# Optimization experiments

Measured on AMD Instinct MI355X. Metric: run time of the kernel, lower is better.

The kernel has to match this reference:

```python
import jax, jax.numpy as jnp
import numpy as np

NUM_CAPS = 8
NITER = 3
TAU = 1.0
N_NODES = 50000
N_EDGES = 800000
D_FEAT = 128


def _l2norm(v):
    # matches torch fn.normalize(dim=-1, eps=1e-12): v / max(||v||, eps)
    n = jnp.linalg.norm(v, axis=-1, keepdims=True)
    return v / jnp.maximum(n, 1e-12)


def setup_inputs() -> dict:
    key = jax.random.key(0)
    k1, k2, k3 = jax.random.split(key, 3)
    x = jax.random.normal(k1, (N_NODES, D_FEAT), dtype=jnp.float32)
    src = jax.random.randint(k2, (N_EDGES,), 0, N_NODES)
    trg = jax.random.randint(k3, (N_EDGES,), 0, N_NODES)
    edge_index = jnp.stack([src, trg], axis=0).astype(jnp.int64)
    return {"x": x, "edge_index": edge_index}


def reference(x, edge_index):
    num_node, num_dim = x.shape
    dpc = num_dim // NUM_CAPS  # dim per capsule
    src, trg = edge_index[0], edge_index[1]

    xc = _l2norm(x.reshape(num_node, NUM_CAPS, dpc))  # [N, C, d]
    z = xc[src]                                        # [E, C, d] gathered source caps
    u = xc
    for _ in range(NITER):
        # per-edge, per-capsule agreement score
        p = jnp.einsum('ecd,ecd->ec', z, u[trg])       # [E, C]
        p = jax.nn.softmax(p / TAU, axis=1)
        msg = z * p[:, :, None]                        # [E, C, d]
        u = jax.ops.segment_sum(msg, trg, num_segments=num_node)  # [N, C, d]
        u = _l2norm(u + xc)
    return u.reshape(num_node, num_dim)
```

## Files before the change

kernel.cpp:

```cpp
#include <hip/hip_runtime.h>
#include <hip/hip_bf16.h>

#define DF   128
#define DPC  16
#define KCAP 64

#define NB_XC    2048
#define NB_BKT   2048
#define NB_ROUTE 1536
#define NB_ZERO  64

__device__ __forceinline__ float cap_sum(float v) {
    v += __shfl_xor(v, 1);
    v += __shfl_xor(v, 2);
    v += __shfl_xor(v, 4);
    return v;
}
__device__ __forceinline__ float bits_lo(unsigned int w) {
    union { unsigned int u; float f; } c; c.u = w << 16; return c.f;
}
__device__ __forceinline__ float bits_hi(unsigned int w) {
    union { unsigned int u; float f; } c; c.u = w & 0xFFFF0000u; return c.f;
}
__device__ __forceinline__ unsigned int f2b_pack(float lo, float hi) {
    __hip_bfloat16 a = __float2bfloat16(lo), b = __float2bfloat16(hi);
    unsigned short ua = *reinterpret_cast<unsigned short*>(&a);
    unsigned short ub = *reinterpret_cast<unsigned short*>(&b);
    return ((unsigned int)ub << 16) | ua;
}
__device__ __forceinline__ float2 load_x2(const void* __restrict__ xraw, int fp32,
                                          int node, int lane) {
    size_t off = (size_t)node * DF + (size_t)lane * 2;
    if (fp32) {
        return *reinterpret_cast<const float2*>((const float*)xraw + off);
    } else {
        unsigned int w = ((const unsigned int*)xraw)[(size_t)node * 64 + lane];
        return make_float2(bits_lo(w), bits_hi(w));
    }
}
__device__ __forceinline__ void proc_pk(const uint4& w0, const uint4& w1,
                                        bool valid, const float* u, float* acc) {
    unsigned ww[8] = {w0.x, w0.y, w0.z, w0.w, w1.x, w1.y, w1.z, w1.w};
    float p = 0.0f;
    #pragma unroll
    for (int q = 0; q < 8; ++q) {
        p = fmaf(bits_lo(ww[q]), u[2*q],   p);
        p = fmaf(bits_hi(ww[q]), u[2*q+1], p);
    }
    float ex = __expf(p);
    float sd = ex;
    sd += __shfl_xor(sd, 1);
    sd += __shfl_xor(sd, 2);
    sd += __shfl_xor(sd, 4);
    float w = valid ? ex * __builtin_amdgcn_rcpf(sd) : 0.0f;
    #pragma unroll
    for (int q = 0; q < 8; ++q) {
        acc[2*q]   = fmaf(w, bits_lo(ww[q]), acc[2*q]);
        acc[2*q+1] = fmaf(w, bits_hi(ww[q]), acc[2*q+1]);
    }
}

__global__ void k_detect_zero(const unsigned int* __restrict__ xw,
                              const unsigned int* __restrict__ ew,
                              int* __restrict__ flags, int* __restrict__ cnt,
                              int zwords) {
    if (blockIdx.x == 0) {
        __shared__ int s_nan, s_zero;
        int tid = threadIdx.x;
        if (tid == 0) { s_nan = 0; s_zero = 0; }
        __syncthreads();
        int cnt_nan = 0;
        for (int i = tid; i < 4096; i += 256) {
            unsigned int lo = xw[i] & 0xFFFFu;
            if ((lo & 0x7F80u) == 0x7F80u) cnt_nan++;
        }
        int cnt_zero = 0;
        for (int i = tid; i < 1024; i += 256) {
            if (ew[2 * i + 1] == 0u) cnt_zero++;
        }
        atomicAdd(&s_nan, cnt_nan);
        atomicAdd(&s_zero, cnt_zero);
        __syncthreads();
        if (tid == 0) {
            flags[0] = (s_nan > 0) ? 1 : 0;
            flags[1] = (s_zero > 512) ? 1 : 0;
        }
    } else {
        int stride = (NB_ZERO - 1) * 256;
        for (int i = (blockIdx.x - 1) * 256 + threadIdx.x; i < zwords; i += stride)
            cnt[i] = 0;
    }
}

__global__ void k_xc(const void* __restrict__ xraw,
                     unsigned int* __restrict__ xcb,
                     const int* __restrict__ flags, int n_nodes) {
    const int fp32 = flags[0];
    const int lane = threadIdx.x & 63;
    const int gw   = (blockIdx.x * blockDim.x + threadIdx.x) >> 6;
    const int nw   = (gridDim.x * blockDim.x) >> 6;
    for (int wid = gw; wid < n_nodes; wid += nw) {
        float2 v = load_x2(xraw, fp32, wid, lane);
        float ss = cap_sum(v.x * v.x + v.y * v.y);
        float scale = 1.0f / fmaxf(sqrtf(ss), 1e-12f);
        int cc = lane >> 3, jp = lane & 7;
        int w = (jp < 4) ? (cc * 4 + jp) : (32 + cc * 4 + (jp - 4));
        xcb[(size_t)wid * 64 + w] = f2b_pack(v.x * scale, v.y * scale);
    }
}

__global__ void k_bucket(const int* __restrict__ ei,
                         int* __restrict__ cnt, int cstr,
                         unsigned short* __restrict__ rows,
                         const int* __restrict__ flags,
                         int n_nodes, int n_edges) {
    const int i64 = flags[1];
    const int gtid = blockIdx.x * blockDim.x + threadIdx.x;
    const int gth  = gridDim.x * blockDim.x;
    for (int e = gtid; e < n_edges; e += gth) {
        int s, t;
        if (i64) {
            long sv = ((const long*)ei)[e];
            long tv = ((const long*)ei)[(size_t)n_edges + e];
            s = (int)sv; t = (int)tv;
        } else {
            s = ei[e]; t = ei[(size_t)n_edges + e];
        }
        if ((unsigned)s < (unsigned)n_nodes && (unsigned)t < (unsigned)n_nodes) {
            int slot = atomicAdd(cnt + (size_t)t * cstr, 1);
            if (slot < KCAP)
                rows[(size_t)t * KCAP + slot] = (unsigned short)s;
        }
    }
}

__global__ void __launch_bounds__(256)
__attribute__((amdgpu_waves_per_eu(8)))
k_route(const unsigned short* __restrict__ rows,
        const unsigned int* __restrict__ xcb,
        const int* __restrict__ cnt, int cstr,
        float* __restrict__ u_out, int n_nodes) {
    __shared__ char smem[4 * 6144];
    const int lane = threadIdx.x & 63;
    char* wbase = smem + (threadIdx.x >> 6) * 6144;
    const int gw = (blockIdx.x * blockDim.x + threadIdx.x) >> 6;
    const int nw = (gridDim.x * blockDim.x) >> 6;
    const int e8 = lane >> 3;
    const int c  = lane & 7;
    const int coff = c * 16;
    const char* __restrict__ xb = (const char*)xcb;

    for (int t = gw; t < n_nodes; t += nw) {
        const unsigned* wrow = (const unsigned*)(rows + (size_t)t * KCAP);
        unsigned rw = wrow[lane & 31];
        int deg = cnt[(size_t)t * cstr];
        deg = __builtin_amdgcn_readfirstlane(deg);
        deg = min(deg, KCAP);

        size_t trow = (size_t)t << 8;
        uint4 t0 = *reinterpret_cast<const uint4*>(xb + trow + coff);
        uint4 t1 = *reinterpret_cast<const uint4*>(xb + trow + 128 + coff);

        auto nid = [&](int s) -> int {
            unsigned wv = __shfl(rw, (lane & 32) | (s >> 1));
            return (int)((s & 1) ? (wv >> 16) : (wv & 0xFFFFu));
        };

        if (deg > 0) {
            int kmax = (min(deg, 24) + 7) >> 3;
            for (int k = 0; k < kmax; ++k) {
                int s  = e8 + 8 * k;
                int sl = (s < deg) ? s : 0;
                int off = nid(sl) << 8;
                const char* ga = xb + off + coff;
                const char* gb = ga + 128;
                __builtin_amdgcn_global_load_lds(
                    (const __attribute__((address_space(1))) unsigned int*)ga,
                    (__attribute__((address_space(3))) unsigned int*)
                        (wbase + k * 2048 + (lane << 4)), 16, 0, 0);
                __builtin_amdgcn_global_load_lds(
                    (const __attribute__((address_space(1))) unsigned int*)gb,
                    (__attribute__((address_space(3))) unsigned int*)
                        (wbase + k * 2048 + 1024 + (lane << 4)), 16, 0, 0);
            }
        }

        unsigned tw[8] = {t0.x, t0.y, t0.z, t0.w, t1.x, t1.y, t1.z, t1.w};
        float ss = 0.0f;
        #pragma unroll
        for (int q = 0; q < 8; ++q) {
            float xl = bits_lo(tw[q]), xh = bits_hi(tw[q]);
            ss = fmaf(xl, xl, ss);
            ss = fmaf(xh, xh, ss);
        }
        float sc = __builtin_amdgcn_rsqf(fmaxf(ss, 1e-24f));
        float u[DPC];
        #pragma unroll
        for (int q = 0; q < 8; ++q) {
            u[2*q]   = bits_lo(tw[q]) * sc;
            u[2*q+1] = bits_hi(tw[q]) * sc;
        }

        asm volatile("s_waitcnt vmcnt(0)" ::: "memory");

        for (int it = 0; it < 3; ++it) {
            asm volatile("" ::: "memory");

            float acc[DPC];
            #pragma unroll
            for (int j = 0; j < DPC; ++j) acc[j] = 0.0f;

            #pragma unroll
            for (int k = 0; k < 3; ++k) {
                if (deg > 8 * k) {
                    uint4 a = *reinterpret_cast<const uint4*>(
                        wbase + k * 2048 + (lane << 4));
                    uint4 b = *reinterpret_cast<const uint4*>(
                        wbase + k * 2048 + 1024 + (lane << 4));
                    proc_pk(a, b, 8 * k + e8 < deg, u, acc);
                }
            }
            if (deg > 24) {
                for (int base = 24; base < deg; base += 8) {
                    int s  = base + e8;
                    int sl = (s < deg) ? s : 0;
                    int off = nid(sl) << 8;
                    uint4 a = *reinterpret_cast<const uint4*>(xb + off + coff);
                    uint4 b = *reinterpret_cast<const uint4*>(xb + off + 128 + coff);
                    proc_pk(a, b, s < deg, u, acc);
                }
            }

            #pragma unroll
            for (int j = 0; j < DPC; ++j) {
                acc[j] += __shfl_xor(acc[j], 8);
                acc[j] += __shfl_xor(acc[j], 16);
                acc[j] += __shfl_xor(acc[j], 32);
            }
            float s2 = 0.0f;
            #pragma unroll
            for (int q = 0; q < 8; ++q) {
                float xl = bits_lo(tw[q]) * sc;
                float xh = bits_hi(tw[q]) * sc;
                u[2*q]   = acc[2*q]   + xl;
                u[2*q+1] = acc[2*q+1] + xh;
                s2 = fmaf(u[2*q],   u[2*q],   s2);
                s2 = fmaf(u[2*q+1], u[2*q+1], s2);
            }
            float sc2 = __builtin_amdgcn_rsqf(fmaxf(s2, 1e-24f));
            #pragma unroll
            for (int j = 0; j < DPC; ++j) u[j] *= sc2;
        }

        if (e8 == 0) {
            float* dst = u_out + (size_t)t * DF + c * DPC;
            #pragma unroll
            for (int j = 0; j < DPC; j += 4)
                *reinterpret_cast<float4*>(dst + j) =
                    make_float4(u[j], u[j+1], u[j+2], u[j+3]);
        }
    }
}

extern "C" void kernel_launch(void* const* d_in, const int* in_sizes, int n_in,
                              void* d_out, int out_size, void* d_ws, size_t ws_size,
                              hipStream_t stream) {
    const void* x  = d_in[0];
    const int*  ei = (const int*)d_in[1];
    const int n_nodes = in_sizes[0] / DF;
    const int n_edges = in_sizes[1] / 2;
    const size_t NC = (size_t)n_nodes * DF;

    unsigned char* p = (unsigned char*)d_ws;
    unsigned int*   xcb  = (unsigned int*)p;   p += NC * 2;
    unsigned short* rows = (unsigned short*)p; p += (size_t)n_nodes * KCAP * 2;
    int*            flags = (int*)p;           p += 128;
    int*            cnt  = (int*)p;
    size_t used  = (size_t)(p - (unsigned char*)d_ws);
    size_t avail = (ws_size > used) ? (ws_size - used) : 0;
    int cstr = 32;
    while (cstr > 1 && (size_t)n_nodes * cstr * sizeof(int) > avail) cstr >>= 1;
    int zwords = n_nodes * cstr;

    float* u_out = (float*)d_out;

    k_detect_zero<<<NB_ZERO, 256, 0, stream>>>(
        (const unsigned int*)x, (const unsigned int*)ei, flags, cnt, zwords);
    k_bucket<<<NB_BKT, 256, 0, stream>>>(ei, cnt, cstr, rows, flags,
                                         n_nodes, n_edges);
    k_xc<<<NB_XC, 256, 0, stream>>>(x, xcb, flags, n_nodes);
    k_route<<<NB_ROUTE, 256, 0, stream>>>(rows, xcb, cnt, cstr, u_out, n_nodes);
}
```

Before: 262.7 us.

## Process two nodes per wave in routing, drop LDS staging, fuse prep kernels

The routing kernel now gives each half-wave its own target node, with 4 edges per pass instead of 8, so low-degree nodes waste fewer lanes. The global-to-LDS staging is replaced by direct global loads of the first 16 neighbours, software-pipelined two at a time and re-read each iteration. The xc normalization and edge bucketing kernels are merged into one launch, and the route grid and waves-per-EU hint are retuned. The cost is re-fetching neighbour rows from cache on every iteration, plus per-half-wave degree divergence, since each wave loops to the larger of its two degrees.

```diff
diff --git a/kernel.cpp b/kernel.cpp
--- a/kernel.cpp
+++ b/kernel.cpp
@@ -4,10 +4,10 @@
 #define DF   128
 #define DPC  16
 #define KCAP 64
-
-#define NB_XC    2048
-#define NB_BKT   2048
-#define NB_ROUTE 1536
+#define RWU  64
+
+#define NB_PREP  2048
+#define NB_ROUTE 1792
 #define NB_ZERO  64
 
 __device__ __forceinline__ float cap_sum(float v) {
@@ -92,9 +92,12 @@
     }
 }
 
-__global__ void k_xc(const void* __restrict__ xraw,
-                     unsigned int* __restrict__ xcb,
-                     const int* __restrict__ flags, int n_nodes) {
+__global__ void k_prep(const void* __restrict__ xraw, unsigned int* __restrict__ xcb,
+                       const int* __restrict__ ei,
+                       int* __restrict__ cnt, int cstr,
+                       unsigned short* __restrict__ rows,
+                       const int* __restrict__ flags,
+                       int n_nodes, int n_edges) {
     const int fp32 = flags[0];
     const int lane = threadIdx.x & 63;
     const int gw   = (blockIdx.x * blockDim.x + threadIdx.x) >> 6;
@@ -107,22 +110,15 @@
         int w = (jp < 4) ? (cc * 4 + jp) : (32 + cc * 4 + (jp - 4));
         xcb[(size_t)wid * 64 + w] = f2b_pack(v.x * scale, v.y * scale);
     }
-}
-
-__global__ void k_bucket(const int* __restrict__ ei,
-                         int* __restrict__ cnt, int cstr,
-                         unsigned short* __restrict__ rows,
-                         const int* __restrict__ flags,
-                         int n_nodes, int n_edges) {
+
     const int i64 = flags[1];
     const int gtid = blockIdx.x * blockDim.x + threadIdx.x;
     const int gth  = gridDim.x * blockDim.x;
     for (int e = gtid; e < n_edges; e += gth) {
         int s, t;
         if (i64) {
-            long sv = ((const long*)ei)[e];
-            long tv = ((const long*)ei)[(size_t)n_edges + e];
-            s = (int)sv; t = (int)tv;
+            s = (int)((const long long*)ei)[e];
+            t = (int)((const long long*)ei)[(size_t)n_edges + e];
         } else {
             s = ei[e]; t = ei[(size_t)n_edges + e];
         }
@@ -135,55 +131,47 @@
 }
 
 __global__ void __launch_bounds__(256)
-__attribute__((amdgpu_waves_per_eu(8)))
+__attribute__((amdgpu_waves_per_eu(7)))
 k_route(const unsigned short* __restrict__ rows,
         const unsigned int* __restrict__ xcb,
         const int* __restrict__ cnt, int cstr,
         float* __restrict__ u_out, int n_nodes) {
-    __shared__ char smem[4 * 6144];
     const int lane = threadIdx.x & 63;
-    char* wbase = smem + (threadIdx.x >> 6) * 6144;
+    const int hl   = lane & 31;
+    const int sl   = (lane >> 3) & 3;
+    const int c    = lane & 7;
+    const int coff = c * 16;
+    const char* __restrict__ xb = (const char*)xcb;
     const int gw = (blockIdx.x * blockDim.x + threadIdx.x) >> 6;
     const int nw = (gridDim.x * blockDim.x) >> 6;
-    const int e8 = lane >> 3;
-    const int c  = lane & 7;
-    const int coff = c * 16;
-    const char* __restrict__ xb = (const char*)xcb;
-
-    for (int t = gw; t < n_nodes; t += nw) {
-        const unsigned* wrow = (const unsigned*)(rows + (size_t)t * KCAP);
-        unsigned rw = wrow[lane & 31];
+    const int npair = (n_nodes + 1) >> 1;
+    const int nmax  = n_nodes - 1;
+
+    for (int pr = gw; pr < npair; pr += nw) {
+        int  tA  = pr * 2;
+        bool wrB = (tA + 1) < n_nodes;
+        int  t   = (lane >= 32 && wrB) ? tA + 1 : tA;
+
+        unsigned rw = ((const unsigned*)(rows + (size_t)t * RWU))[hl];
         int deg = cnt[(size_t)t * cstr];
-        deg = __builtin_amdgcn_readfirstlane(deg);
         deg = min(deg, KCAP);
 
         size_t trow = (size_t)t << 8;
         uint4 t0 = *reinterpret_cast<const uint4*>(xb + trow + coff);
         uint4 t1 = *reinterpret_cast<const uint4*>(xb + trow + 128 + coff);
 
+        int dm = max(deg, __shfl_xor(deg, 32));
+        int km = __builtin_amdgcn_readfirstlane((dm + 3) >> 2);
+
         auto nid = [&](int s) -> int {
             unsigned wv = __shfl(rw, (lane & 32) | (s >> 1));
-            return (int)((s & 1) ? (wv >> 16) : (wv & 0xFFFFu));
+            int id = (int)((s & 1) ? (wv >> 16) : (wv & 0xFFFFu));
+            return min(id, nmax);
         };
-
-        if (deg > 0) {
-            int kmax = (min(deg, 24) + 7) >> 3;
-            for (int k = 0; k < kmax; ++k) {
-                int s  = e8 + 8 * k;
-                int sl = (s < deg) ? s : 0;
-                int off = nid(sl) << 8;
-                const char* ga = xb + off + coff;
-                const char* gb = ga + 128;
-                __builtin_amdgcn_global_load_lds(
-                    (const __attribute__((address_space(1))) unsigned int*)ga,
-                    (__attribute__((address_space(3))) unsigned int*)
-                        (wbase + k * 2048 + (lane << 4)), 16, 0, 0);
-                __builtin_amdgcn_global_load_lds(
-                    (const __attribute__((address_space(1))) unsigned int*)gb,
-                    (__attribute__((address_space(3))) unsigned int*)
-                        (wbase + k * 2048 + 1024 + (lane << 4)), 16, 0, 0);
-            }
-        }
+        int s0 = sl,      off0 = (deg > 0)  ? (nid(s0 < deg ? s0 : 0) << 8) : 0;
+        int s1 = sl + 4,  off1 = (deg > 4)  ? (nid(s1 < deg ? s1 : 0) << 8) : 0;
+        int s2 = sl + 8,  off2 = (deg > 8)  ? (nid(s2 < deg ? s2 : 0) << 8) : 0;
+        int s3 = sl + 12, off3 = (deg > 12) ? (nid(s3 < deg ? s3 : 0) << 8) : 0;
 
         unsigned tw[8] = {t0.x, t0.y, t0.z, t0.w, t1.x, t1.y, t1.z, t1.w};
         float ss = 0.0f;
@@ -201,41 +189,47 @@
             u[2*q+1] = bits_hi(tw[q]) * sc;
         }
 
-        asm volatile("s_waitcnt vmcnt(0)" ::: "memory");
-
         for (int it = 0; it < 3; ++it) {
+            asm volatile("" : "+v"(rw));
             asm volatile("" ::: "memory");
 
             float acc[DPC];
             #pragma unroll
             for (int j = 0; j < DPC; ++j) acc[j] = 0.0f;
 
-            #pragma unroll
-            for (int k = 0; k < 3; ++k) {
-                if (deg > 8 * k) {
-                    uint4 a = *reinterpret_cast<const uint4*>(
-                        wbase + k * 2048 + (lane << 4));
-                    uint4 b = *reinterpret_cast<const uint4*>(
-                        wbase + k * 2048 + 1024 + (lane << 4));
-                    proc_pk(a, b, 8 * k + e8 < deg, u, acc);
-                }
-            }
-            if (deg > 24) {
-                for (int base = 24; base < deg; base += 8) {
-                    int s  = base + e8;
-                    int sl = (s < deg) ? s : 0;
-                    int off = nid(sl) << 8;
-                    uint4 a = *reinterpret_cast<const uint4*>(xb + off + coff);
-                    uint4 b = *reinterpret_cast<const uint4*>(xb + off + 128 + coff);
-                    proc_pk(a, b, s < deg, u, acc);
-                }
+            uint4 a0, b0, a1, b1;
+            if (km > 0) {
+                a0 = *reinterpret_cast<const uint4*>(xb + off0 + coff);
+                b0 = *reinterpret_cast<const uint4*>(xb + off0 + 128 + coff);
+            }
+            if (km > 1) {
+                a1 = *reinterpret_cast<const uint4*>(xb + off1 + coff);
+                b1 = *reinterpret_cast<const uint4*>(xb + off1 + 128 + coff);
+            }
+            if (km > 0) proc_pk(a0, b0, s0 < deg, u, acc);
+            if (km > 2) {
+                a0 = *reinterpret_cast<const uint4*>(xb + off2 + coff);
+                b0 = *reinterpret_cast<const uint4*>(xb + off2 + 128 + coff);
+            }
+            if (km > 1) proc_pk(a1, b1, s1 < deg, u, acc);
+            if (km > 3) {
+                a1 = *reinterpret_cast<const uint4*>(xb + off3 + coff);
+                b1 = *reinterpret_cast<const uint4*>(xb + off3 + 128 + coff);
+            }
+            if (km > 2) proc_pk(a0, b0, s2 < deg, u, acc);
+            if (km > 3) proc_pk(a1, b1, s3 < deg, u, acc);
+            for (int k = 4; k < km; ++k) {
+                int s  = 4 * k + sl;
+                int off = nid(s < deg ? s : 0) << 8;
+                uint4 a = *reinterpret_cast<const uint4*>(xb + off + coff);
+                uint4 b = *reinterpret_cast<const uint4*>(xb + off + 128 + coff);
+                proc_pk(a, b, s < deg, u, acc);
             }
 
             #pragma unroll
             for (int j = 0; j < DPC; ++j) {
                 acc[j] += __shfl_xor(acc[j], 8);
                 acc[j] += __shfl_xor(acc[j], 16);
-                acc[j] += __shfl_xor(acc[j], 32);
             }
             float s2 = 0.0f;
             #pragma unroll
@@ -252,7 +246,7 @@
             for (int j = 0; j < DPC; ++j) u[j] *= sc2;
         }
 
-        if (e8 == 0) {
+        if (sl == 0 && (lane < 32 || wrB)) {
             float* dst = u_out + (size_t)t * DF + c * DPC;
             #pragma unroll
             for (int j = 0; j < DPC; j += 4)
@@ -286,8 +280,7 @@
 
     k_detect_zero<<<NB_ZERO, 256, 0, stream>>>(
         (const unsigned int*)x, (const unsigned int*)ei, flags, cnt, zwords);
-    k_bucket<<<NB_BKT, 256, 0, stream>>>(ei, cnt, cstr, rows, flags,
-                                         n_nodes, n_edges);
-    k_xc<<<NB_XC, 256, 0, stream>>>(x, xcb, flags, n_nodes);
+    k_prep<<<NB_PREP, 256, 0, stream>>>(x, xcb, ei, cnt, cstr, rows, flags,
+                                        n_nodes, n_edges);
     k_route<<<NB_ROUTE, 256, 0, stream>>>(rows, xcb, cnt, cstr, u_out, n_nodes);
 }
```

After: 407.9 us. +55.3%, slower.

## Fuse normalize and bucket kernels; register-cache neighbor caps with one wave per node

Applied to the files above, without the earlier changes.

Merges the capsule-normalize kernel and the edge-bucketing kernel into a single prep launch, which removes one launch and its gap. The routing kernel drops the LDS staging via global_load_lds and the persistent grid-stride loop. Each wave now handles one node and keeps its first 16 neighbors' capsules in registers across the three iterations, reloading the rest from global memory. This trades LDS reuse for higher register pressure and more global reloads on high-degree nodes, but may raise occupancy since it no longer allocates shared memory.

```diff
diff --git a/kernel.cpp b/kernel.cpp
--- a/kernel.cpp
+++ b/kernel.cpp
@@ -4,10 +4,10 @@
 #define DF   128
 #define DPC  16
 #define KCAP 64
-
-#define NB_XC    2048
-#define NB_BKT   2048
-#define NB_ROUTE 1536
+#define RWU  64
+#define WPB  4
+
+#define NB_PREP  2048
 #define NB_ZERO  64
 
 __device__ __forceinline__ float cap_sum(float v) {
@@ -92,9 +92,12 @@
     }
 }
 
-__global__ void k_xc(const void* __restrict__ xraw,
-                     unsigned int* __restrict__ xcb,
-                     const int* __restrict__ flags, int n_nodes) {
+__global__ void k_prep(const void* __restrict__ xraw, unsigned int* __restrict__ xcb,
+                       const int* __restrict__ ei,
+                       int* __restrict__ cnt, int cstr,
+                       unsigned short* __restrict__ rows,
+                       const int* __restrict__ flags,
+                       int n_nodes, int n_edges) {
     const int fp32 = flags[0];
     const int lane = threadIdx.x & 63;
     const int gw   = (blockIdx.x * blockDim.x + threadIdx.x) >> 6;
@@ -107,158 +110,124 @@
         int w = (jp < 4) ? (cc * 4 + jp) : (32 + cc * 4 + (jp - 4));
         xcb[(size_t)wid * 64 + w] = f2b_pack(v.x * scale, v.y * scale);
     }
-}
-
-__global__ void k_bucket(const int* __restrict__ ei,
-                         int* __restrict__ cnt, int cstr,
-                         unsigned short* __restrict__ rows,
-                         const int* __restrict__ flags,
-                         int n_nodes, int n_edges) {
+
     const int i64 = flags[1];
     const int gtid = blockIdx.x * blockDim.x + threadIdx.x;
     const int gth  = gridDim.x * blockDim.x;
     for (int e = gtid; e < n_edges; e += gth) {
         int s, t;
         if (i64) {
-            long sv = ((const long*)ei)[e];
-            long tv = ((const long*)ei)[(size_t)n_edges + e];
-            s = (int)sv; t = (int)tv;
+            s = (int)((const long long*)ei)[e];
+            t = (int)((const long long*)ei)[(size_t)n_edges + e];
         } else {
             s = ei[e]; t = ei[(size_t)n_edges + e];
         }
         if ((unsigned)s < (unsigned)n_nodes && (unsigned)t < (unsigned)n_nodes) {
             int slot = atomicAdd(cnt + (size_t)t * cstr, 1);
             if (slot < KCAP)
-                rows[(size_t)t * KCAP + slot] = (unsigned short)s;
+                __builtin_nontemporal_store(
+                    (unsigned short)s, rows + (size_t)t * KCAP + slot);
         }
     }
 }
 
 __global__ void __launch_bounds__(256)
-__attribute__((amdgpu_waves_per_eu(8)))
 k_route(const unsigned short* __restrict__ rows,
         const unsigned int* __restrict__ xcb,
         const int* __restrict__ cnt, int cstr,
         float* __restrict__ u_out, int n_nodes) {
-    __shared__ char smem[4 * 6144];
-    const int lane = threadIdx.x & 63;
-    char* wbase = smem + (threadIdx.x >> 6) * 6144;
-    const int gw = (blockIdx.x * blockDim.x + threadIdx.x) >> 6;
-    const int nw = (gridDim.x * blockDim.x) >> 6;
+    int t    = (blockIdx.x * blockDim.x + threadIdx.x) >> 6;
+    int lane = threadIdx.x & 63;
+    if (t >= n_nodes) return;
     const int e8 = lane >> 3;
     const int c  = lane & 7;
     const int coff = c * 16;
     const char* __restrict__ xb = (const char*)xcb;
 
-    for (int t = gw; t < n_nodes; t += nw) {
-        const unsigned* wrow = (const unsigned*)(rows + (size_t)t * KCAP);
-        unsigned rw = wrow[lane & 31];
-        int deg = cnt[(size_t)t * cstr];
-        deg = __builtin_amdgcn_readfirstlane(deg);
-        deg = min(deg, KCAP);
-
-        size_t trow = (size_t)t << 8;
-        uint4 t0 = *reinterpret_cast<const uint4*>(xb + trow + coff);
-        uint4 t1 = *reinterpret_cast<const uint4*>(xb + trow + 128 + coff);
-
-        auto nid = [&](int s) -> int {
-            unsigned wv = __shfl(rw, (lane & 32) | (s >> 1));
-            return (int)((s & 1) ? (wv >> 16) : (wv & 0xFFFFu));
-        };
-
-        if (deg > 0) {
-            int kmax = (min(deg, 24) + 7) >> 3;
-            for (int k = 0; k < kmax; ++k) {
-                int s  = e8 + 8 * k;
-                int sl = (s < deg) ? s : 0;
-                int off = nid(sl) << 8;
-                const char* ga = xb + off + coff;
-                const char* gb = ga + 128;
-                __builtin_amdgcn_global_load_lds(
-                    (const __attribute__((address_space(1))) unsigned int*)ga,
-                    (__attribute__((address_space(3))) unsigned int*)
-                        (wbase + k * 2048 + (lane << 4)), 16, 0, 0);
-                __builtin_amdgcn_global_load_lds(
-                    (const __attribute__((address_space(1))) unsigned int*)gb,
-                    (__attribute__((address_space(3))) unsigned int*)
-                        (wbase + k * 2048 + 1024 + (lane << 4)), 16, 0, 0);
-            }
-        }
-
-        unsigned tw[8] = {t0.x, t0.y, t0.z, t0.w, t1.x, t1.y, t1.z, t1.w};
-        float ss = 0.0f;
+    unsigned rw = ((const unsigned*)(rows + (size_t)t * RWU))[lane & 31];
+
+    size_t trow = (size_t)t << 8;
+    uint4 t0 = *reinterpret_cast<const uint4*>(xb + trow + coff);
+    uint4 t1 = *reinterpret_cast<const uint4*>(xb + trow + 128 + coff);
+    int deg = cnt[(size_t)t * cstr];
+    deg = __builtin_amdgcn_readfirstlane(deg);
+    deg = min(deg, KCAP);
+
+    auto nid = [&](int s) -> int {
+        unsigned wv = __shfl(rw, (lane & 32) | (s >> 1));
+        return (int)((s & 1) ? (wv >> 16) : (wv & 0xFFFFu));
+    };
+    auto ldc = [&](int k, uint4& a, uint4& b) {
+        int s  = e8 + 8 * k;
+        int sl = (s < deg) ? s : 0;
+        int off = nid(sl) << 8;
+        a = *reinterpret_cast<const uint4*>(xb + off + coff);
+        b = *reinterpret_cast<const uint4*>(xb + off + 128 + coff);
+    };
+
+    uint4 k0a, k0b, k1a, k1b;
+    if (deg > 0) ldc(0, k0a, k0b);
+    if (deg > 8) ldc(1, k1a, k1b);
+
+    unsigned tw[8] = {t0.x, t0.y, t0.z, t0.w, t1.x, t1.y, t1.z, t1.w};
+    float ss = 0.0f;
+    #pragma unroll
+    for (int q = 0; q < 8; ++q) {
+        float xl = bits_lo(tw[q]), xh = bits_hi(tw[q]);
+        ss = fmaf(xl, xl, ss);
+        ss = fmaf(xh, xh, ss);
+    }
+    float sc = __builtin_amdgcn_rsqf(fmaxf(ss, 1e-24f));
+    float u[DPC];
+    #pragma unroll
+    for (int q = 0; q < 8; ++q) {
+        u[2*q]   = bits_lo(tw[q]) * sc;
+        u[2*q+1] = bits_hi(tw[q]) * sc;
+    }
+
+    for (int it = 0; it < 3; ++it) {
+        float acc[DPC];
+        #pragma unroll
+        for (int j = 0; j < DPC; ++j) acc[j] = 0.0f;
+
+        if (deg > 0) proc_pk(k0a, k0b, e8 < deg,     u, acc);
+        if (deg > 8) proc_pk(k1a, k1b, 8 + e8 < deg, u, acc);
+        for (int base = 16; base < deg; base += 8) {
+            int s  = base + e8;
+            int sl = (s < deg) ? s : 0;
+            int off = nid(sl) << 8;
+            uint4 a = *reinterpret_cast<const uint4*>(xb + off + coff);
+            uint4 b = *reinterpret_cast<const uint4*>(xb + off + 128 + coff);
+            proc_pk(a, b, s < deg, u, acc);
+        }
+
+        #pragma unroll
+        for (int j = 0; j < DPC; ++j) {
+            acc[j] += __shfl_xor(acc[j], 8);
+            acc[j] += __shfl_xor(acc[j], 16);
+            acc[j] += __shfl_xor(acc[j], 32);
+        }
+        float s2 = 0.0f;
         #pragma unroll
         for (int q = 0; q < 8; ++q) {
-            float xl = bits_lo(tw[q]), xh = bits_hi(tw[q]);
-            ss = fmaf(xl, xl, ss);
-            ss = fmaf(xh, xh, ss);
-        }
-        float sc = __builtin_amdgcn_rsqf(fmaxf(ss, 1e-24f));
-        float u[DPC];
-        #pragma unroll
-        for (int q = 0; q < 8; ++q) {
-            u[2*q]   = bits_lo(tw[q]) * sc;
-            u[2*q+1] = bits_hi(tw[q]) * sc;
-        }
-
-        asm volatile("s_waitcnt vmcnt(0)" ::: "memory");
-
-        for (int it = 0; it < 3; ++it) {
-            asm volatile("" ::: "memory");
-
-            float acc[DPC];
-            #pragma unroll
-            for (int j = 0; j < DPC; ++j) acc[j] = 0.0f;
-
-            #pragma unroll
-            for (int k = 0; k < 3; ++k) {
-                if (deg > 8 * k) {
-                    uint4 a = *reinterpret_cast<const uint4*>(
-                        wbase + k * 2048 + (lane << 4));
-                    uint4 b = *reinterpret_cast<const uint4*>(
-                        wbase + k * 2048 + 1024 + (lane << 4));
-                    proc_pk(a, b, 8 * k + e8 < deg, u, acc);
-                }
-            }
-            if (deg > 24) {
-                for (int base = 24; base < deg; base += 8) {
-                    int s  = base + e8;
-                    int sl = (s < deg) ? s : 0;
-                    int off = nid(sl) << 8;
-                    uint4 a = *reinterpret_cast<const uint4*>(xb + off + coff);
-                    uint4 b = *reinterpret_cast<const uint4*>(xb + off + 128 + coff);
-                    proc_pk(a, b, s < deg, u, acc);
-                }
-            }
-
-            #pragma unroll
-            for (int j = 0; j < DPC; ++j) {
-                acc[j] += __shfl_xor(acc[j], 8);
-                acc[j] += __shfl_xor(acc[j], 16);
-                acc[j] += __shfl_xor(acc[j], 32);
-            }
-            float s2 = 0.0f;
-            #pragma unroll
-            for (int q = 0; q < 8; ++q) {
-                float xl = bits_lo(tw[q]) * sc;
-                float xh = bits_hi(tw[q]) * sc;
-                u[2*q]   = acc[2*q]   + xl;
-                u[2*q+1] = acc[2*q+1] + xh;
-                s2 = fmaf(u[2*q],   u[2*q],   s2);
-                s2 = fmaf(u[2*q+1], u[2*q+1], s2);
-            }
-            float sc2 = __builtin_amdgcn_rsqf(fmaxf(s2, 1e-24f));
-            #pragma unroll
-            for (int j = 0; j < DPC; ++j) u[j] *= sc2;
-        }
-
-        if (e8 == 0) {
-            float* dst = u_out + (size_t)t * DF + c * DPC;
-            #pragma unroll
-            for (int j = 0; j < DPC; j += 4)
-                *reinterpret_cast<float4*>(dst + j) =
-                    make_float4(u[j], u[j+1], u[j+2], u[j+3]);
-        }
+            float xl = bits_lo(tw[q]) * sc;
+            float xh = bits_hi(tw[q]) * sc;
+            u[2*q]   = acc[2*q]   + xl;
+            u[2*q+1] = acc[2*q+1] + xh;
+            s2 = fmaf(u[2*q],   u[2*q],   s2);
+            s2 = fmaf(u[2*q+1], u[2*q+1], s2);
+        }
+        float sc2 = __builtin_amdgcn_rsqf(fmaxf(s2, 1e-24f));
+        #pragma unroll
+        for (int j = 0; j < DPC; ++j) u[j] *= sc2;
+    }
+
+    if (e8 == 0) {
+        float* dst = u_out + (size_t)t * DF + c * DPC;
+        #pragma unroll
+        for (int j = 0; j < DPC; j += 4)
+            *reinterpret_cast<float4*>(dst + j) =
+                make_float4(u[j], u[j+1], u[j+2], u[j+3]);
     }
 }
 
@@ -284,10 +253,11 @@
 
     float* u_out = (float*)d_out;
 
+    const int nb_route = (n_nodes + WPB - 1) / WPB;
+
     k_detect_zero<<<NB_ZERO, 256, 0, stream>>>(
         (const unsigned int*)x, (const unsigned int*)ei, flags, cnt, zwords);
-    k_bucket<<<NB_BKT, 256, 0, stream>>>(ei, cnt, cstr, rows, flags,
-                                         n_nodes, n_edges);
-    k_xc<<<NB_XC, 256, 0, stream>>>(x, xcb, flags, n_nodes);
-    k_route<<<NB_ROUTE, 256, 0, stream>>>(rows, xcb, cnt, cstr, u_out, n_nodes);
-}
+    k_prep<<<NB_PREP, 256, 0, stream>>>(x, xcb, ei, cnt, cstr, rows, flags,
+                                        n_nodes, n_edges);
+    k_route<<<nb_route, 256, 0, stream>>>(rows, xcb, cnt, cstr, u_out, n_nodes);
+}
```

Result: faster. 252.8 us (-3.8%).
